# Kernel optimization log

Measured on AMD Instinct MI355X. Metric: run time of the kernel, lower is better.

Reference implementation:

```python
import jax, jax.numpy as jnp
import numpy as np


def _rnn_scan(x_pre, W_hh, b_hh, h0):
    # x_pre: [S, B, H] precomputed input projection; returns stacked h: [S, B, H]
    def step(h, xp):
        h = jnp.tanh(xp + h @ W_hh.T + b_hh)
        return h, h
    _, hs = jax.lax.scan(step, h0, x_pre)
    return hs


def setup_inputs() -> dict:
    key = jax.random.key(0)
    ks = jax.random.split(key, 12)
    B, S, E, H, V = 16, 256, 512, 1024, 32000
    sE, sH = 1.0 / np.sqrt(E), 1.0 / np.sqrt(H)
    return {
        "x_ids": jax.random.randint(ks[0], (B, S), 0, V),
        "emb": jax.random.normal(ks[1], (V, E), jnp.float32),
        "W_ih1": jax.random.normal(ks[2], (H, E), jnp.float32) * sE,
        "b_ih1": jax.random.normal(ks[3], (H,), jnp.float32) * sH,
        "W_hh1": jax.random.normal(ks[4], (H, H), jnp.float32) * sH,
        "b_hh1": jax.random.normal(ks[5], (H,), jnp.float32) * sH,
        "W_ih2": jax.random.normal(ks[6], (H, H), jnp.float32) * sH,
        "b_ih2": jax.random.normal(ks[7], (H,), jnp.float32) * sH,
        "W_hh2": jax.random.normal(ks[8], (H, H), jnp.float32) * sH,
        "b_hh2": jax.random.normal(ks[9], (H,), jnp.float32) * sH,
        "W_fc": jax.random.normal(ks[10], (V, H), jnp.float32) * sH,
        "b_fc": jax.random.normal(ks[11], (V,), jnp.float32) * sH,
    }


def reference(x_ids, emb, W_ih1, b_ih1, W_hh1, b_hh1, W_ih2, b_ih2, W_hh2, b_hh2, W_fc, b_fc):
    B, S = x_ids.shape
    H = W_hh1.shape[0]
    x = emb[x_ids]  # [B, S, E]
    # layer 1: precompute input projection for all steps, scan over time
    x1 = jnp.einsum('bse,he->sbh', x, W_ih1) + b_ih1  # [S, B, H]
    h0 = jnp.zeros((B, H), x.dtype)
    h1s = _rnn_scan(x1, W_hh1, b_hh1, h0)  # [S, B, H]
    # layer 2
    x2 = jnp.einsum('sbh,gh->sbg', h1s, W_ih2) + b_ih2
    h2s = _rnn_scan(x2, W_hh2, b_hh2, h0)  # [S, B, H]
    # per-step fc + softmax, vectorized
    logits = jnp.einsum('sbh,vh->bsv', h2s, W_fc) + b_fc  # [B, S, V]
    return jax.nn.softmax(logits, axis=-1)
```

## Files before the change

kernel.cpp:

```cpp
#include <hip/hip_runtime.h>
#include <cstdint>
#include <cstddef>
#include <math.h>

typedef unsigned short u16;
typedef __attribute__((ext_vector_type(4))) float f32x4;
typedef __attribute__((ext_vector_type(8))) short s16x8;
typedef __attribute__((ext_vector_type(8))) unsigned short u16x8;
typedef __attribute__((ext_vector_type(4))) unsigned short u16x4;
typedef __attribute__((ext_vector_type(4))) unsigned u32x4;

#define B_ 16
#define S_ 256
#define E_ 512
#define H_ 1024
#define V_ 32000
#define M_TOK (S_*B_)
#define BH (B_*H_)
#define NT_FC 250
#define MT_FC 32

__device__ __forceinline__ u16 f2bf(float f) {
  union { float f; unsigned u; } x; x.f = f;
  unsigned r = x.u + 0x7fffu + ((x.u >> 16) & 1u);
  return (u16)(r >> 16);
}
__device__ __forceinline__ float bf2f(u16 x) {
  union { unsigned u; float f; } c; c.u = ((unsigned)x) << 16; return c.f;
}

__device__ __forceinline__ void sc_load16(s16x8& d, const u16* p) {
  asm volatile("global_load_dwordx4 %0, %1, off sc0 sc1" : "=v"(d) : "v"(p));
}
__device__ __forceinline__ void sc_load16u(u32x4& d, const u16* p) {
  asm volatile("global_load_dwordx4 %0, %1, off sc0 sc1" : "=v"(d) : "v"(p));
}
__device__ __forceinline__ void sc_load8w(u16x4& d, const u16* p) {
  asm volatile("global_load_dwordx2 %0, %1, off sc0 sc1\n\ts_waitcnt vmcnt(0)"
               : "=v"(d) : "v"(p) : "memory");
}
__device__ __forceinline__ int sc_load4w(const int* p) {
  int d;
  asm volatile("global_load_dword %0, %1, off sc0 sc1\n\ts_waitcnt vmcnt(0)"
               : "=v"(d) : "v"(p) : "memory");
  return d;
}
__device__ __forceinline__ void sc_store8(u16* p, u16x4 v) {
  asm volatile("global_store_dwordx2 %0, %1, off sc0 sc1" :: "v"(p), "v"(v) : "memory");
}
__device__ __forceinline__ void sc_store4(int* p, int v) {
  asm volatile("global_store_dword %0, %1, off sc0 sc1" :: "v"(p), "v"(v) : "memory");
}
__device__ __forceinline__ void wait_vm0() {
  asm volatile("s_waitcnt vmcnt(0)" ::: "memory");
}

__global__ __launch_bounds__(256)
void k_cvt_all(const float* s0, u16* d0, int n0,
               const float* s1, u16* d1, int n1,
               const float* s2, u16* d2, int n2,
               const float* s3, u16* d3, int n3,
               const float* s4, u16* d4, int n4)
{
  const int total = n0 + n1 + n2 + n3 + n4;
  for (int i = blockIdx.x*256 + threadIdx.x; i < total; i += gridDim.x*256) {
    const float* s; u16* d; int j = i;
    if (j < n0) { s = s0; d = d0; }
    else { j -= n0;
      if (j < n1) { s = s1; d = d1; }
      else { j -= n1;
        if (j < n2) { s = s2; d = d2; }
        else { j -= n2;
          if (j < n3) { s = s3; d = d3; }
          else { j -= n3; s = s4; d = d4; } } } }
    float4 v = reinterpret_cast<const float4*>(s)[j];
    ushort4 o;
    o.x = f2bf(v.x); o.y = f2bf(v.y); o.z = f2bf(v.z); o.w = f2bf(v.w);
    reinterpret_cast<ushort4*>(d)[j] = o;
  }
}

__global__ __launch_bounds__(256) void k_embed(const int* __restrict__ ids,
                                               const float* __restrict__ emb,
                                               u16* __restrict__ A1) {
  int g = blockIdx.x*256 + threadIdx.x;
  int m = g >> 6;
  int c = g & 63;
  int s = m >> 4, b = m & 15;
  int id = ids[b*S_ + s];
  const float4* src = reinterpret_cast<const float4*>(emb + (size_t)id*E_ + (size_t)c*8);
  float4 v0 = src[0], v1 = src[1];
  u16x8 o;
  o[0]=f2bf(v0.x); o[1]=f2bf(v0.y); o[2]=f2bf(v0.z); o[3]=f2bf(v0.w);
  o[4]=f2bf(v1.x); o[5]=f2bf(v1.y); o[6]=f2bf(v1.z); o[7]=f2bf(v1.w);
  *reinterpret_cast<u16x8*>(A1 + (size_t)m*E_ + (size_t)c*8) = o;
}

#define BM 128
#define BN 128
#define BK 32

__device__ __forceinline__ void gload_lds16(const u16* g, u16* l) {
  __builtin_amdgcn_global_load_lds(
      (const __attribute__((address_space(1))) void*)g,
      (__attribute__((address_space(3))) void*)l,
      16, 0, 0);
}

template<int FCMODE>
__global__ __launch_bounds__(256)
void k_gemm(const u16* __restrict__ A, const u16* __restrict__ Bw,
            float* __restrict__ C, const float* __restrict__ bias,
            int M, int N, int K)
{
  __shared__ u16 lA[2][BM*BK];
  __shared__ u16 lB[2][BN*BK];
  const int tid = threadIdx.x;
  const int l = tid & 63, w = tid >> 6;

  const int nwg = gridDim.x * gridDim.y;
  int d = blockIdx.y * gridDim.x + blockIdx.x;
  int tt = (d & 7) * (nwg >> 3) + (d >> 3);
  const int n0 = (tt / gridDim.y) * BN;
  const int m0 = (tt % gridDim.y) * BM;

  const int wr = w >> 1, wc = w & 1;

  const int L0 = (w*2+0)*64 + l;
  const int L1 = (w*2+1)*64 + l;
  const int r0 = L0 >> 2, r1 = L1 >> 2;
  const int c0 = (L0 & 3) ^ ((r0 >> 1) & 3);
  const int c1 = (L1 & 3) ^ ((r1 >> 1) & 3);
  const u16* gA0 = A  + (size_t)(m0 + r0)*K + c0*8;
  const u16* gA1 = A  + (size_t)(m0 + r1)*K + c1*8;
  const u16* gB0 = Bw + (size_t)(n0 + r0)*K + c0*8;
  const u16* gB1 = Bw + (size_t)(n0 + r1)*K + c1*8;

  const int fr = l & 15;
  const int xc = (l >> 4) ^ ((fr >> 1) & 3);
  int aoff[4], boff[4];
#pragma unroll
  for (int f = 0; f < 4; ++f) {
    aoff[f] = (wr*64 + f*16 + fr) * BK + xc*8;
    boff[f] = (wc*64 + f*16 + fr) * BK + xc*8;
  }

  f32x4 acc[4][4] = {};
  const int KT = K / BK;

  gload_lds16(gA0, &lA[0][(w*2+0)*512]);
  gload_lds16(gA1, &lA[0][(w*2+1)*512]);
  gload_lds16(gB0, &lB[0][(w*2+0)*512]);
  gload_lds16(gB1, &lB[0][(w*2+1)*512]);
  __syncthreads();

  for (int kt = 0; kt < KT; ++kt) {
    const int buf = kt & 1;
    if (kt + 1 < KT) {
      const int koff = (kt+1)*BK;
      gload_lds16(gA0 + koff, &lA[buf^1][(w*2+0)*512]);
      gload_lds16(gA1 + koff, &lA[buf^1][(w*2+1)*512]);
      gload_lds16(gB0 + koff, &lB[buf^1][(w*2+0)*512]);
      gload_lds16(gB1 + koff, &lB[buf^1][(w*2+1)*512]);
    }
    s16x8 af[4], bq[4];
#pragma unroll
    for (int f = 0; f < 4; ++f) af[f] = *reinterpret_cast<const s16x8*>(&lA[buf][aoff[f]]);
#pragma unroll
    for (int f = 0; f < 4; ++f) bq[f] = *reinterpret_cast<const s16x8*>(&lB[buf][boff[f]]);
#pragma unroll
    for (int fm = 0; fm < 4; ++fm)
#pragma unroll
      for (int fn = 0; fn < 4; ++fn)
        acc[fm][fn] = __builtin_amdgcn_mfma_f32_16x16x32_bf16(af[fm], bq[fn], acc[fm][fn], 0, 0, 0);
    __syncthreads();
  }

  const int rowb = (l >> 4) * 4;
  const int colb = l & 15;
#pragma unroll
  for (int fm = 0; fm < 4; ++fm) {
#pragma unroll
    for (int fn = 0; fn < 4; ++fn) {
      const int col = n0 + wc*64 + fn*16 + colb;
#pragma unroll
      for (int r = 0; r < 4; ++r) {
        const int row = m0 + wr*64 + fm*16 + rowb + r;
        float v = acc[fm][fn][r];
        if (FCMODE == 2) {
          ((u16*)C)[(size_t)row*N + col] = f2bf(v);
        } else {
          C[(size_t)row*N + col] = v;
        }
      }
    }
  }
}

__device__ __forceinline__ void fc_tile(const u16* __restrict__ A, const u16* __restrict__ Bw,
                                        float* __restrict__ C, const float* __restrict__ bias,
                                        float2* __restrict__ stat,
                                        int m0, int n0, u16* smem)
{
  const int tid = threadIdx.x;
  const int l = tid & 63, w = tid >> 6;
  const int wr = w >> 1, wc = w & 1;
  const int nt = n0 / BN;
  u16* lA = smem;
  u16* lB = smem + 8192;

  const int L0 = (w*2+0)*64 + l;
  const int L1 = (w*2+1)*64 + l;
  const int r0 = L0 >> 2, r1 = L1 >> 2;
  const int c0 = (L0 & 3) ^ ((r0 >> 1) & 3);
  const int c1 = (L1 & 3) ^ ((r1 >> 1) & 3);
  const u16* gA0 = A  + (size_t)(m0 + r0)*H_ + c0*8;
  const u16* gA1 = A  + (size_t)(m0 + r1)*H_ + c1*8;
  const u16* gB0 = Bw + (size_t)(n0 + r0)*H_ + c0*8;
  const u16* gB1 = Bw + (size_t)(n0 + r1)*H_ + c1*8;

  const int fr = l & 15;
  const int xc = (l >> 4) ^ ((fr >> 1) & 3);
  int aoff[4], boff[4];
#pragma unroll
  for (int f = 0; f < 4; ++f) {
    aoff[f] = (wr*64 + f*16 + fr) * BK + xc*8;
    boff[f] = (wc*64 + f*16 + fr) * BK + xc*8;
  }

  f32x4 acc[4][4] = {};

  gload_lds16(gA0, lA + (w*2+0)*512);
  gload_lds16(gA1, lA + (w*2+1)*512);
  gload_lds16(gB0, lB + (w*2+0)*512);
  gload_lds16(gB1, lB + (w*2+1)*512);
  __syncthreads();

  for (int kt = 0; kt < 32; ++kt) {
    const int buf = kt & 1;
    if (kt + 1 < 32) {
      const int koff = (kt+1)*BK;
      gload_lds16(gA0 + koff, lA + (buf^1)*4096 + (w*2+0)*512);
      gload_lds16(gA1 + koff, lA + (buf^1)*4096 + (w*2+1)*512);
      gload_lds16(gB0 + koff, lB + (buf^1)*4096 + (w*2+0)*512);
      gload_lds16(gB1 + koff, lB + (buf^1)*4096 + (w*2+1)*512);
    }
    s16x8 af[4], bq[4];
#pragma unroll
    for (int f = 0; f < 4; ++f) af[f] = *reinterpret_cast<const s16x8*>(lA + buf*4096 + aoff[f]);
#pragma unroll
    for (int f = 0; f < 4; ++f) bq[f] = *reinterpret_cast<const s16x8*>(lB + buf*4096 + boff[f]);
#pragma unroll
    for (int fm = 0; fm < 4; ++fm)
#pragma unroll
      for (int fn = 0; fn < 4; ++fn)
        acc[fm][fn] = __builtin_amdgcn_mfma_f32_16x16x32_bf16(af[fm], bq[fn], acc[fm][fn], 0, 0, 0);
    __syncthreads();
  }

  const int rowb = (l >> 4) * 4;
  const int colb = l & 15;

#pragma unroll
  for (int fm = 0; fm < 4; ++fm) {
#pragma unroll
    for (int fn = 0; fn < 4; ++fn) {
      const int col = n0 + wc*64 + fn*16 + colb;
      const float bv = bias[col];
#pragma unroll
      for (int r = 0; r < 4; ++r) {
        const int row = m0 + wr*64 + fm*16 + rowb + r;
        const int b = row & 15, s = row >> 4;
        acc[fm][fn][r] += bv;
        C[((size_t)(b*S_ + s))*V_ + col] = acc[fm][fn][r];
      }
    }
  }

  float2* stats = reinterpret_cast<float2*>(smem);
#pragma unroll
  for (int fm = 0; fm < 4; ++fm) {
#pragma unroll
    for (int r = 0; r < 4; ++r) {
      float mx = fmaxf(fmaxf(acc[fm][0][r], acc[fm][1][r]),
                       fmaxf(acc[fm][2][r], acc[fm][3][r]));
#pragma unroll
      for (int o = 1; o <= 8; o <<= 1) mx = fmaxf(mx, __shfl_xor(mx, o));
      float sm = __expf(acc[fm][0][r]-mx) + __expf(acc[fm][1][r]-mx)
               + __expf(acc[fm][2][r]-mx) + __expf(acc[fm][3][r]-mx);
#pragma unroll
      for (int o = 1; o <= 8; o <<= 1) sm += __shfl_xor(sm, o);
      if (colb == 0) {
        const int j = wr*64 + fm*16 + rowb + r;
        stats[j*2 + wc] = make_float2(mx, sm);
      }
    }
  }
  __syncthreads();
  if (tid < 128) {
    float2 h0 = stats[tid*2 + 0], h1 = stats[tid*2 + 1];
    float mx = fmaxf(h0.x, h1.x);
    float sm = h0.y*__expf(h0.x - mx) + h1.y*__expf(h1.x - mx);
    stat[(size_t)(m0 + tid)*NT_FC + nt] = make_float2(mx, sm);
  }
}

__global__ __launch_bounds__(256)
void k_mega(const u16* __restrict__ Whh1, const u16* __restrict__ Wih2,
            const u16* __restrict__ Whh2, const u16* __restrict__ x1b,
            const float* __restrict__ bih1, const float* __restrict__ bhh1,
            const float* __restrict__ bih2, const float* __restrict__ bhh2,
            u16* __restrict__ h1s, u16* __restrict__ u2s, u16* __restrict__ h2s,
            int* __restrict__ s1, int* __restrict__ su, int* __restrict__ s2,
            const u16* __restrict__ Wfcb, const float* __restrict__ bfc,
            float* __restrict__ out, float2* __restrict__ stat,
            int* __restrict__ prog2, int* __restrict__ done)
{
  __shared__ u16 smem[16384];
  const int bid = blockIdx.x;
  const int tid = threadIdx.x;

  if (bid < 48) {
    const int l = tid & 63, w = tid >> 6;
    const int role = bid >> 4;
    const int blk  = bid & 15;
    const int rowA = blk*64 + w*16 + (l & 15);
    const int kc = l >> 4;
    const int bcol = l & 15;
    const int i0 = blk*64 + w*16 + kc*4;
    const int jme = (tid & 127) >> 3;

    const u16* Wsel = (role == 0) ? Whh1 : (role == 1) ? Wih2 : Whh2;
    s16x8 wf[32];
    {
      const u16* wp = Wsel + (size_t)rowA*H_ + kc*8;
#pragma unroll
      for (int ks = 0; ks < 32; ++ks) wf[ks] = *reinterpret_cast<const s16x8*>(wp + ks*32);
    }

    auto stage = [&](const u16* src, const int* sentrow) {
      while (sc_load4w(sentrow + jme) != 0) __builtin_amdgcn_s_sleep(2);
      s16x8 stg[8];
#pragma unroll
      for (int r = 0; r < 8; ++r) sc_load16(stg[r], src + (size_t)(tid + r*256)*8);
      wait_vm0();
#pragma unroll
      for (int r = 0; r < 8; ++r) {
        int idx8 = tid + r*256;
        int bt = idx8 >> 7, c8 = idx8 & 127;
        *reinterpret_cast<s16x8*>(reinterpret_cast<char*>(smem) +
            bt*2048 + ((c8*16) ^ ((bt & 7) << 4))) = stg[r];
      }
    };

    const int swz = (bcol & 7) << 4;
    auto hfrag = [&](int ks) -> s16x8 {
      return *reinterpret_cast<const s16x8*>(
          reinterpret_cast<const char*>(smem) + bcol*2048 + (((kc*16) + ks*64) ^ swz));
    };
    auto mfma32 = [&](f32x4& a0, f32x4& a1, f32x4& a2, f32x4& a3) {
#pragma unroll
      for (int ks = 0; ks < 32; ks += 4) {
        a0 = __builtin_amdgcn_mfma_f32_16x16x32_bf16(wf[ks+0], hfrag(ks+0), a0, 0, 0, 0);
        a1 = __builtin_amdgcn_mfma_f32_16x16x32_bf16(wf[ks+1], hfrag(ks+1), a1, 0, 0, 0);
        a2 = __builtin_amdgcn_mfma_f32_16x16x32_bf16(wf[ks+2], hfrag(ks+2), a2, 0, 0, 0);
        a3 = __builtin_amdgcn_mfma_f32_16x16x32_bf16(wf[ks+3], hfrag(ks+3), a3, 0, 0, 0);
      }
    };

    if (role == 0) {
      float bc[4];
#pragma unroll
      for (int r = 0; r < 4; ++r) bc[r] = bih1[i0+r] + bhh1[i0+r];
      for (int t = 0; t < S_; ++t) {
        f32x4 a0 = {}, a1 = {}, a2 = {}, a3 = {};
        if (t > 0) {
          stage(h1s + (size_t)(t-1)*BH, s1 + (t-1)*16);
          __syncthreads();
          mfma32(a0, a1, a2, a3);
        }
        u16x4 xr = *reinterpret_cast<const u16x4*>(x1b + (size_t)(t*B_ + bcol)*H_ + i0);
        f32x4 tot = (a0 + a1) + (a2 + a3);
        u16x4 o;
        o[0] = f2bf(tanhf(tot[0] + bf2f(xr[0]) + bc[0]));
        o[1] = f2bf(tanhf(tot[1] + bf2f(xr[1]) + bc[1]));
        o[2] = f2bf(tanhf(tot[2] + bf2f(xr[2]) + bc[2]));
        o[3] = f2bf(tanhf(tot[3] + bf2f(xr[3]) + bc[3]));
        sc_store8(h1s + (size_t)(t*B_ + bcol)*H_ + i0, o);
        wait_vm0();
        __syncthreads();
        if (tid == 0) sc_store4(s1 + t*16 + blk, 0);
      }
    } else if (role == 1) {
      float bc[4];
#pragma unroll
      for (int r = 0; r < 4; ++r) bc[r] = bih2[i0+r] + bhh2[i0+r];
      for (int t = 0; t < S_; ++t) {
        stage(h1s + (size_t)t*BH, s1 + t*16);
        __syncthreads();
        f32x4 a0 = {}, a1 = {}, a2 = {}, a3 = {};
        mfma32(a0, a1, a2, a3);
        f32x4 tot = (a0 + a1) + (a2 + a3);
        u16x4 o;
        o[0] = f2bf(tot[0] + bc[0]);
        o[1] = f2bf(tot[1] + bc[1]);
        o[2] = f2bf(tot[2] + bc[2]);
        o[3] = f2bf(tot[3] + bc[3]);
        sc_store8(u2s + (size_t)(t*B_ + bcol)*H_ + i0, o);
        wait_vm0();
        __syncthreads();
        if (tid == 0) sc_store4(su + t*16 + blk, 0);
      }
    } else {
      for (int t = 0; t < S_; ++t) {
        if (tid == 0) {
          while (sc_load4w(su + t*16 + blk) != 0) __builtin_amdgcn_s_sleep(2);
        }
        if (t > 0) stage(h2s + (size_t)(t-1)*BH, s2 + (t-1)*16);
        __syncthreads();
        u16x4 uv;
        sc_load8w(uv, u2s + (size_t)(t*B_ + bcol)*H_ + i0);
        f32x4 a0 = {}, a1 = {}, a2 = {}, a3 = {};
        if (t > 0) mfma32(a0, a1, a2, a3);
        f32x4 tot = (a0 + a1) + (a2 + a3);
        u16x4 o;
        o[0] = f2bf(tanhf(tot[0] + bf2f(uv[0])));
        o[1] = f2bf(tanhf(tot[1] + bf2f(uv[1])));
        o[2] = f2bf(tanhf(tot[2] + bf2f(uv[2])));
        o[3] = f2bf(tanhf(tot[3] + bf2f(uv[3])));
        sc_store8(h2s + (size_t)(t*B_ + bcol)*H_ + i0, o);
        wait_vm0();
        __syncthreads();
        if (tid == 0) {
          sc_store4(s2 + t*16 + blk, 0);
          sc_store4(prog2 + blk, t + 1);
        }
      }
    }
    return;
  }

  const int q = bid - 48;
  if (q >= MT_FC * NT_FC) return;
  const int mt = q / NT_FC;
  const int nt = q - mt * NT_FC;
  const unsigned need = (unsigned)((mt + 1) * 8);

  __shared__ int s_ok;
  if (tid == 0) {
    int ok = 0;
    const u16* pp = (const u16*)prog2;
    for (int it = 0; it < 2500; ++it) {
      u32x4 pa, pb, pc, pd;
      sc_load16u(pa, pp); sc_load16u(pb, pp + 8);
      sc_load16u(pc, pp + 16); sc_load16u(pd, pp + 24);
      wait_vm0();
      unsigned m0 = pa[0] < pa[1] ? pa[0] : pa[1];
      unsigned m1 = pa[2] < pa[3] ? pa[2] : pa[3];
      unsigned m2 = pb[0] < pb[1] ? pb[0] : pb[1];
      unsigned m3 = pb[2] < pb[3] ? pb[2] : pb[3];
      unsigned m4 = pc[0] < pc[1] ? pc[0] : pc[1];
      unsigned m5 = pc[2] < pc[3] ? pc[2] : pc[3];
      unsigned m6 = pd[0] < pd[1] ? pd[0] : pd[1];
      unsigned m7 = pd[2] < pd[3] ? pd[2] : pd[3];
      m0 = m0 < m1 ? m0 : m1;  m2 = m2 < m3 ? m2 : m3;
      m4 = m4 < m5 ? m4 : m5;  m6 = m6 < m7 ? m6 : m7;
      m0 = m0 < m2 ? m0 : m2;  m4 = m4 < m6 ? m4 : m6;
      unsigned mn = m0 < m4 ? m0 : m4;
      if (mn >= need) { ok = 1; break; }
      __builtin_amdgcn_s_sleep(32);
    }
    s_ok = ok;
  }
  __syncthreads();
  if (!s_ok) return;

  fc_tile(h2s, Wfcb, out, bfc, stat, mt*BM, nt*BN, smem);
  if (tid == 0) done[q] = 1;
}

__global__ __launch_bounds__(256)
void k_fc_cleanup(const u16* __restrict__ h2s, const u16* __restrict__ Wfcb,
                  const float* __restrict__ bfc, float* __restrict__ out,
                  float2* __restrict__ stat, const int* __restrict__ done)
{
  __shared__ u16 smem[16384];
  const int q = blockIdx.x;
  if (done[q]) return;
  const int mt = q / NT_FC;
  const int nt = q - mt * NT_FC;
  fc_tile(h2s, Wfcb, out, bfc, stat, mt*BM, nt*BN, smem);
}

__global__ __launch_bounds__(256)
void k_norm(float* __restrict__ out, const float2* __restrict__ stat) {
  const int gw = (blockIdx.x*256 + threadIdx.x) >> 6;
  const int l = threadIdx.x & 63;
  const int b = gw & 15, s = gw >> 4;
  float* row = out + ((size_t)b*S_ + s)*V_;
  const float2* st = stat + (size_t)gw*NT_FC;
  float m = -3.4e38f, sum = 0.f;
  for (int i = l; i < NT_FC; i += 64) {
    float2 e = st[i];
    float nm = fmaxf(m, e.x);
    sum = sum*__expf(m - nm) + e.y*__expf(e.x - nm);
    m = nm;
  }
#pragma unroll
  for (int o = 32; o; o >>= 1) {
    float m2 = __shfl_xor(m, o), s2 = __shfl_xor(sum, o);
    float nm = fmaxf(m, m2);
    sum = sum*__expf(m - nm) + s2*__expf(m2 - nm);
    m = nm;
  }
  const float inv = 1.f / sum;
  for (int it = 0; it < 125; ++it) {
    float4 x = reinterpret_cast<const float4*>(row)[it*64 + l];
    float4 p;
    p.x = __expf(x.x - m)*inv; p.y = __expf(x.y - m)*inv;
    p.z = __expf(x.z - m)*inv; p.w = __expf(x.w - m)*inv;
    reinterpret_cast<float4*>(row)[it*64 + l] = p;
  }
}

extern "C" void kernel_launch(void* const* d_in, const int* in_sizes, int n_in,
                              void* d_out, int out_size, void* d_ws, size_t ws_size,
                              hipStream_t stream) {
  (void)in_sizes; (void)n_in; (void)out_size; (void)ws_size;
  const int*   x_ids = (const int*)  d_in[0];
  const float* emb   = (const float*)d_in[1];
  const float* Wih1  = (const float*)d_in[2];
  const float* bih1  = (const float*)d_in[3];
  const float* Whh1  = (const float*)d_in[4];
  const float* bhh1  = (const float*)d_in[5];
  const float* Wih2  = (const float*)d_in[6];
  const float* bih2  = (const float*)d_in[7];
  const float* Whh2  = (const float*)d_in[8];
  const float* bhh2  = (const float*)d_in[9];
  const float* Wfc   = (const float*)d_in[10];
  const float* bfc   = (const float*)d_in[11];
  float* out = (float*)d_out;

  char* ws = (char*)d_ws;
  size_t off = 0;
  auto alloc = [&](size_t bytes) {
    char* p = ws + off; off += (bytes + 255) & ~(size_t)255; return p;
  };
  int* sent   = (int*) alloc(3 * S_ * 16 * 4);
  const int CTRL_INTS = 16 + MT_FC*NT_FC;
  int* ctrl   = (int*) alloc(CTRL_INTS * 4);
  float2* stat= (float2*)alloc((size_t)M_TOK * NT_FC * 8);
  u16* Wfcb   = (u16*) alloc((size_t)V_*H_*2);
  u16* Whh1b  = (u16*) alloc((size_t)H_*H_*2);
  u16* Wih2b  = (u16*) alloc((size_t)H_*H_*2);
  u16* Whh2b  = (u16*) alloc((size_t)H_*H_*2);
  u16* x1b    = (u16*) alloc((size_t)M_TOK*H_*2);
  u16* h1s    = (u16*) alloc((size_t)M_TOK*H_*2);
  u16* u2s    = (u16*) alloc((size_t)M_TOK*H_*2);
  u16* h2s    = (u16*) alloc((size_t)M_TOK*H_*2);
  u16* A1     = (u16*) alloc((size_t)M_TOK*E_*2);
  u16* Wih1b  = (u16*) alloc((size_t)H_*E_*2);
  int* s1 = sent, *su = sent + S_*16, *s2 = sent + 2*S_*16;
  int* prog2 = ctrl;
  int* done  = ctrl + 16;

  k_cvt_all<<<2048, 256, 0, stream>>>(Wih1, Wih1b, H_*E_/4,
                                      Whh1, Whh1b, H_*H_/4,
                                      Wih2, Wih2b, H_*H_/4,
                                      Whh2, Whh2b, H_*H_/4,
                                      Wfc,  Wfcb,  V_*H_/4);
  k_embed<<<M_TOK*64/256, 256, 0, stream>>>(x_ids, emb, A1);

  k_gemm<2><<<dim3(H_/BN, M_TOK/BM), 256, 0, stream>>>(A1, Wih1b, (float*)x1b, nullptr, M_TOK, H_, E_);

  hipMemsetAsync(sent, 0xFF, 3 * S_ * 16 * 4, stream);
  hipMemsetAsync(ctrl, 0, CTRL_INTS * 4, stream);

  k_mega<<<48 + MT_FC*NT_FC, 256, 0, stream>>>(
      Whh1b, Wih2b, Whh2b, x1b, bih1, bhh1, bih2, bhh2,
      h1s, u2s, h2s, s1, su, s2, Wfcb, bfc, out, stat, prog2, done);

  k_fc_cleanup<<<MT_FC*NT_FC, 256, 0, stream>>>(h2s, Wfcb, bfc, out, stat, done);
  k_norm<<<M_TOK/4, 256, 0, stream>>>(out, stat);
}
```

Measured before the change: 1.600 ms.

## Overlap W_fc bf16 conversion with recurrence and drop max-subtraction in softmax

Moves the large W_fc fp32-to-bf16 conversion out of the upfront conversion kernel into extra blocks of the persistent mega-kernel, where it runs alongside the serial RNN recurrence. FC tiles wait on a per-tile conversion flag. Separately, the softmax partial statistics drop the running max and keep only sums of exp(logit), which removes shuffles, exps and half of the stat traffic. Dropping the max risks overflow for large logits, so correctness now depends on the logits staying small, as they do for these input scales.

```diff
diff --git a/kernel.cpp b/kernel.cpp
--- a/kernel.cpp
+++ b/kernel.cpp
@@ -19,6 +19,7 @@
 #define BH (B_*H_)
 #define NT_FC 250
 #define MT_FC 32
+#define NCVT 250
 
 __device__ __forceinline__ u16 f2bf(float f) {
   union { float f; unsigned u; } x; x.f = f;
@@ -56,13 +57,12 @@
 }
 
 __global__ __launch_bounds__(256)
-void k_cvt_all(const float* s0, u16* d0, int n0,
-               const float* s1, u16* d1, int n1,
-               const float* s2, u16* d2, int n2,
-               const float* s3, u16* d3, int n3,
-               const float* s4, u16* d4, int n4)
+void k_cvt_small(const float* s0, u16* d0, int n0,
+                 const float* s1, u16* d1, int n1,
+                 const float* s2, u16* d2, int n2,
+                 const float* s3, u16* d3, int n3)
 {
-  const int total = n0 + n1 + n2 + n3 + n4;
+  const int total = n0 + n1 + n2 + n3;
   for (int i = blockIdx.x*256 + threadIdx.x; i < total; i += gridDim.x*256) {
     const float* s; u16* d; int j = i;
     if (j < n0) { s = s0; d = d0; }
@@ -70,9 +70,7 @@
       if (j < n1) { s = s1; d = d1; }
       else { j -= n1;
         if (j < n2) { s = s2; d = d2; }
-        else { j -= n2;
-          if (j < n3) { s = s3; d = d3; }
-          else { j -= n3; s = s4; d = d4; } } } }
+        else { j -= n2; s = s3; d = d3; } } }
     float4 v = reinterpret_cast<const float4*>(s)[j];
     ushort4 o;
     o.x = f2bf(v.x); o.y = f2bf(v.y); o.z = f2bf(v.z); o.w = f2bf(v.w);
@@ -199,7 +197,7 @@
 
 __device__ __forceinline__ void fc_tile(const u16* __restrict__ A, const u16* __restrict__ Bw,
                                         float* __restrict__ C, const float* __restrict__ bias,
-                                        float2* __restrict__ stat,
+                                        float* __restrict__ stat,
                                         int m0, int n0, u16* smem)
 {
   const int tid = threadIdx.x;
@@ -277,31 +275,24 @@
     }
   }
 
-  float2* stats = reinterpret_cast<float2*>(smem);
+  float* stats = reinterpret_cast<float*>(smem);
 #pragma unroll
   for (int fm = 0; fm < 4; ++fm) {
 #pragma unroll
     for (int r = 0; r < 4; ++r) {
-      float mx = fmaxf(fmaxf(acc[fm][0][r], acc[fm][1][r]),
-                       fmaxf(acc[fm][2][r], acc[fm][3][r]));
-#pragma unroll
-      for (int o = 1; o <= 8; o <<= 1) mx = fmaxf(mx, __shfl_xor(mx, o));
-      float sm = __expf(acc[fm][0][r]-mx) + __expf(acc[fm][1][r]-mx)
-               + __expf(acc[fm][2][r]-mx) + __expf(acc[fm][3][r]-mx);
+      float sm = __expf(acc[fm][0][r]) + __expf(acc[fm][1][r])
+               + __expf(acc[fm][2][r]) + __expf(acc[fm][3][r]);
 #pragma unroll
       for (int o = 1; o <= 8; o <<= 1) sm += __shfl_xor(sm, o);
       if (colb == 0) {
         const int j = wr*64 + fm*16 + rowb + r;
-        stats[j*2 + wc] = make_float2(mx, sm);
+        stats[j*2 + wc] = sm;
       }
     }
   }
   __syncthreads();
   if (tid < 128) {
-    float2 h0 = stats[tid*2 + 0], h1 = stats[tid*2 + 1];
-    float mx = fmaxf(h0.x, h1.x);
-    float sm = h0.y*__expf(h0.x - mx) + h1.y*__expf(h1.x - mx);
-    stat[(size_t)(m0 + tid)*NT_FC + nt] = make_float2(mx, sm);
+    stat[(size_t)(m0 + tid)*NT_FC + nt] = stats[tid*2 + 0] + stats[tid*2 + 1];
   }
 }
 
@@ -312,9 +303,10 @@
             const float* __restrict__ bih2, const float* __restrict__ bhh2,
             u16* __restrict__ h1s, u16* __restrict__ u2s, u16* __restrict__ h2s,
             int* __restrict__ s1, int* __restrict__ su, int* __restrict__ s2,
-            const u16* __restrict__ Wfcb, const float* __restrict__ bfc,
-            float* __restrict__ out, float2* __restrict__ stat,
-            int* __restrict__ prog2, int* __restrict__ done)
+            const float* __restrict__ Wfc, u16* __restrict__ Wfcb,
+            const float* __restrict__ bfc,
+            float* __restrict__ out, float* __restrict__ stat,
+            int* __restrict__ prog2, int* __restrict__ done, int* __restrict__ cvtdone)
 {
   __shared__ u16 smem[16384];
   const int bid = blockIdx.x;
@@ -440,7 +432,25 @@
     return;
   }
 
-  const int q = bid - 48;
+  if (bid < 48 + NCVT) {
+    const int nt = bid - 48;
+    const float* src = Wfc  + (size_t)nt*128*H_;
+    u16*         dst = Wfcb + (size_t)nt*128*H_;
+#pragma unroll 4
+    for (int i = 0; i < 128; ++i) {
+      const int idx = tid + i*256;
+      float4 v = reinterpret_cast<const float4*>(src)[idx];
+      u16x4 o;
+      o[0] = f2bf(v.x); o[1] = f2bf(v.y); o[2] = f2bf(v.z); o[3] = f2bf(v.w);
+      sc_store8(dst + (size_t)idx*4, o);
+    }
+    wait_vm0();
+    __syncthreads();
+    if (tid == 0) sc_store4(cvtdone + nt, 1);
+    return;
+  }
+
+  const int q = bid - 48 - NCVT;
   if (q >= MT_FC * NT_FC) return;
   const int mt = q / NT_FC;
   const int nt = q - mt * NT_FC;
@@ -467,7 +477,7 @@
       m4 = m4 < m5 ? m4 : m5;  m6 = m6 < m7 ? m6 : m7;
       m0 = m0 < m2 ? m0 : m2;  m4 = m4 < m6 ? m4 : m6;
       unsigned mn = m0 < m4 ? m0 : m4;
-      if (mn >= need) { ok = 1; break; }
+      if (mn >= need && sc_load4w(cvtdone + nt) != 0) { ok = 1; break; }
       __builtin_amdgcn_s_sleep(32);
     }
     s_ok = ok;
@@ -482,7 +492,7 @@
 __global__ __launch_bounds__(256)
 void k_fc_cleanup(const u16* __restrict__ h2s, const u16* __restrict__ Wfcb,
                   const float* __restrict__ bfc, float* __restrict__ out,
-                  float2* __restrict__ stat, const int* __restrict__ done)
+                  float* __restrict__ stat, const int* __restrict__ done)
 {
   __shared__ u16 smem[16384];
   const int q = blockIdx.x;
@@ -493,32 +503,22 @@
 }
 
 __global__ __launch_bounds__(256)
-void k_norm(float* __restrict__ out, const float2* __restrict__ stat) {
+void k_norm(float* __restrict__ out, const float* __restrict__ stat) {
   const int gw = (blockIdx.x*256 + threadIdx.x) >> 6;
   const int l = threadIdx.x & 63;
   const int b = gw & 15, s = gw >> 4;
   float* row = out + ((size_t)b*S_ + s)*V_;
-  const float2* st = stat + (size_t)gw*NT_FC;
-  float m = -3.4e38f, sum = 0.f;
-  for (int i = l; i < NT_FC; i += 64) {
-    float2 e = st[i];
-    float nm = fmaxf(m, e.x);
-    sum = sum*__expf(m - nm) + e.y*__expf(e.x - nm);
-    m = nm;
-  }
-#pragma unroll
-  for (int o = 32; o; o >>= 1) {
-    float m2 = __shfl_xor(m, o), s2 = __shfl_xor(sum, o);
-    float nm = fmaxf(m, m2);
-    sum = sum*__expf(m - nm) + s2*__expf(m2 - nm);
-    m = nm;
-  }
+  const float* st = stat + (size_t)gw*NT_FC;
+  float sum = 0.f;
+  for (int i = l; i < NT_FC; i += 64) sum += st[i];
+#pragma unroll
+  for (int o = 32; o; o >>= 1) sum += __shfl_xor(sum, o);
   const float inv = 1.f / sum;
   for (int it = 0; it < 125; ++it) {
     float4 x = reinterpret_cast<const float4*>(row)[it*64 + l];
     float4 p;
-    p.x = __expf(x.x - m)*inv; p.y = __expf(x.y - m)*inv;
-    p.z = __expf(x.z - m)*inv; p.w = __expf(x.w - m)*inv;
+    p.x = __expf(x.x)*inv; p.y = __expf(x.y)*inv;
+    p.z = __expf(x.z)*inv; p.w = __expf(x.w)*inv;
     reinterpret_cast<float4*>(row)[it*64 + l] = p;
   }
 }
@@ -547,9 +547,9 @@
     char* p = ws + off; off += (bytes + 255) & ~(size_t)255; return p;
   };
   int* sent   = (int*) alloc(3 * S_ * 16 * 4);
-  const int CTRL_INTS = 16 + MT_FC*NT_FC;
+  const int CTRL_INTS = 16 + MT_FC*NT_FC + NCVT;
   int* ctrl   = (int*) alloc(CTRL_INTS * 4);
-  float2* stat= (float2*)alloc((size_t)M_TOK * NT_FC * 8);
+  float* stat = (float*)alloc((size_t)M_TOK * NT_FC * 4);
   u16* Wfcb   = (u16*) alloc((size_t)V_*H_*2);
   u16* Whh1b  = (u16*) alloc((size_t)H_*H_*2);
   u16* Wih2b  = (u16*) alloc((size_t)H_*H_*2);
@@ -561,14 +561,14 @@
   u16* A1     = (u16*) alloc((size_t)M_TOK*E_*2);
   u16* Wih1b  = (u16*) alloc((size_t)H_*E_*2);
   int* s1 = sent, *su = sent + S_*16, *s2 = sent + 2*S_*16;
-  int* prog2 = ctrl;
-  int* done  = ctrl + 16;
-
-  k_cvt_all<<<2048, 256, 0, stream>>>(Wih1, Wih1b, H_*E_/4,
-                                      Whh1, Whh1b, H_*H_/4,
-                                      Wih2, Wih2b, H_*H_/4,
-                                      Whh2, Whh2b, H_*H_/4,
-                                      Wfc,  Wfcb,  V_*H_/4);
+  int* prog2   = ctrl;
+  int* done    = ctrl + 16;
+  int* cvtdone = done + MT_FC*NT_FC;
+
+  k_cvt_small<<<1024, 256, 0, stream>>>(Wih1, Wih1b, H_*E_/4,
+                                        Whh1, Whh1b, H_*H_/4,
+                                        Wih2, Wih2b, H_*H_/4,
+                                        Whh2, Whh2b, H_*H_/4);
   k_embed<<<M_TOK*64/256, 256, 0, stream>>>(x_ids, emb, A1);
 
   k_gemm<2><<<dim3(H_/BN, M_TOK/BM), 256, 0, stream>>>(A1, Wih1b, (float*)x1b, nullptr, M_TOK, H_, E_);
@@ -576,9 +576,9 @@
   hipMemsetAsync(sent, 0xFF, 3 * S_ * 16 * 4, stream);
   hipMemsetAsync(ctrl, 0, CTRL_INTS * 4, stream);
 
-  k_mega<<<48 + MT_FC*NT_FC, 256, 0, stream>>>(
+  k_mega<<<48 + NCVT + MT_FC*NT_FC, 256, 0, stream>>>(
       Whh1b, Wih2b, Whh2b, x1b, bih1, bhh1, bih2, bhh2,
-      h1s, u2s, h2s, s1, su, s2, Wfcb, bfc, out, stat, prog2, done);
+      h1s, u2s, h2s, s1, su, s2, Wfc, Wfcb, bfc, out, stat, prog2, done, cvtdone);
 
   k_fc_cleanup<<<MT_FC*NT_FC, 256, 0, stream>>>(h2s, Wfcb, bfc, out, stat, done);
   k_norm<<<M_TOK/4, 256, 0, stream>>>(out, stat);
```

Result: no change. 1.570 ms (-1.9%).
